# Optimization experiments

Measured on AMD Instinct MI355X. Metric: run time of the kernel, lower is better.

Reference implementation:

```python
import jax, jax.numpy as jnp
import numpy as np

EMB_DIM = 1024
ATT_DIM = 1024
N_HEADS = 16
HEAD_DIM = ATT_DIM // N_HEADS
ROPE_THETA = 10000.0


def setup_inputs() -> dict:
    key = jax.random.key(0)
    k1, k2, k3 = jax.random.split(key, 3)
    B, S = 2, 2048
    x = jax.random.normal(k1, (B, S, EMB_DIM), dtype=jnp.float32)
    # nn.Linear weights stored as [in, out] for x @ W
    W_qkv = jax.random.normal(k2, (EMB_DIM, 3 * ATT_DIM), dtype=jnp.float32) / np.sqrt(EMB_DIM)
    W_out = jax.random.normal(k3, (ATT_DIM, EMB_DIM), dtype=jnp.float32) / np.sqrt(ATT_DIM)
    return {"x": x, "W_qkv": W_qkv, "W_out": W_out}


def _rope_cos_sin(seq_len, dim, dtype):
    # rotary-embedding-torch: freqs over even indices, repeated interleaved
    inv_freq = 1.0 / (ROPE_THETA ** (jnp.arange(0, dim, 2, dtype=jnp.float32) / dim))
    t = jnp.arange(seq_len, dtype=jnp.float32)
    freqs = t[:, None] * inv_freq[None, :]            # [S, dim/2]
    freqs = jnp.repeat(freqs, 2, axis=-1)             # [S, dim] interleaved
    return jnp.cos(freqs).astype(dtype), jnp.sin(freqs).astype(dtype)


def _rotate_half(x):
    # interleaved pairs: (x0, x1) -> (-x1, x0)
    xr = x.reshape(x.shape[:-1] + (x.shape[-1] // 2, 2))
    x1, x2 = xr[..., 0], xr[..., 1]
    return jnp.stack([-x2, x1], axis=-1).reshape(x.shape)


def _apply_rope(x, cos, sin):
    # x: [B, H, S, D]; cos/sin: [S, D]
    return x * cos[None, None] + _rotate_half(x) * sin[None, None]


def reference(x, W_qkv, W_out):
    B, S, _ = x.shape
    qkv = x @ W_qkv                                   # [B, S, 3*ATT]
    qkv = qkv.reshape(B, S, 3, N_HEADS, HEAD_DIM)
    qkv = jnp.moveaxis(qkv, 3, 1)                     # [B, H, S, 3, D]
    q, k, v = qkv[..., 0, :], qkv[..., 1, :], qkv[..., 2, :]

    cos, sin = _rope_cos_sin(S, HEAD_DIM, x.dtype)
    q = _apply_rope(q, cos, sin)
    k = _apply_rope(k, cos, sin)

    scale = 1.0 / np.sqrt(HEAD_DIM)
    scores = jnp.einsum("bhqd,bhkd->bhqk", q, k) * scale
    attn = jax.nn.softmax(scores, axis=-1)
    out = jnp.einsum("bhqk,bhkd->bhqd", attn, v)      # [B, H, S, D]
    out = jnp.moveaxis(out, 1, 2).reshape(B, S, ATT_DIM)
    return out @ W_out                                # [B, S, EMB_DIM]
```

## Files before the change

### kernel.cpp

```cpp
#include <hip/hip_runtime.h>
#include <cstdint>
#include <cstddef>

typedef unsigned short u16;
typedef __bf16 bf16x8 __attribute__((ext_vector_type(8)));
typedef float f32x4 __attribute__((ext_vector_type(4)));
typedef unsigned int u32x4 __attribute__((ext_vector_type(4)));

#define DEVI __device__ __forceinline__

constexpr int SEQ = 2048, NH = 16, HD = 64, EMB = 1024, N3 = 3072, MROWS = 4096;

DEVI u16 f2bf(float f) {
    union { float f; unsigned u; } x; x.f = f;
    unsigned r = (x.u + 0x7fffu + ((x.u >> 16) & 1u)) >> 16;
    return (u16)r;
}

DEVI f32x4 mfma16(bf16x8 a, bf16x8 b, f32x4 c) {
    return __builtin_amdgcn_mfma_f32_16x16x32_bf16(a, b, c, 0, 0, 0);
}

DEVI float exp2_raw(float x) {
    float r;
    asm("v_exp_f32 %0, %1" : "=v"(r) : "v"(x));
    return r;
}

#define GLDS16(g, l)                                                          \
    __builtin_amdgcn_global_load_lds(                                         \
        (__attribute__((address_space(1))) void*)(g),                         \
        (__attribute__((address_space(3))) void*)(l), 16, 0, 0)

#define GWAIT4 asm volatile("s_waitcnt vmcnt(4)" ::: "memory")
#define GWAIT0 asm volatile("s_waitcnt vmcnt(0)" ::: "memory")
#define RBAR                                                                  \
    do {                                                                      \
        __builtin_amdgcn_sched_barrier(0);                                    \
        __builtin_amdgcn_s_barrier();                                         \
        __builtin_amdgcn_sched_barrier(0);                                    \
    } while (0)

__global__ __launch_bounds__(256) void prep_k(const float* __restrict__ x,
                                              const float* __restrict__ wqk,
                                              const float* __restrict__ wo,
                                              u16* __restrict__ xb, u16* __restrict__ wqkvT,
                                              u16* __restrict__ woutT, float2* __restrict__ tab) {
    __shared__ float tile[64][65];
    int bid = blockIdx.x, tid = threadIdx.x;
    if (bid < 4096) {
        int i = bid * 256 + tid;
        float4 v = ((const float4*)x)[i];
        ushort4 o;
        o.x = f2bf(v.x); o.y = f2bf(v.y); o.z = f2bf(v.z); o.w = f2bf(v.w);
        ((ushort4*)xb)[i] = o;
    } else if (bid < 5120) {
        const float* in; u16* out; int N, bx, by;
        if (bid < 4864) { in = wqk; out = wqkvT; N = 3072; int bb = bid - 4096; bx = bb % 48; by = bb / 48; }
        else            { in = wo;  out = woutT; N = 1024; int bb = bid - 4864; bx = bb % 16; by = bb / 16; }
        const int K = 1024;
        int k0 = by * 64, n0 = bx * 64;
        for (int i = 0; i < 16; i++) {
            int idx = i * 256 + tid;
            int r = idx >> 6, c = idx & 63;
            tile[r][c] = in[(size_t)(k0 + r) * N + n0 + c];
        }
        __syncthreads();
        for (int i = 0; i < 16; i++) {
            int idx = i * 256 + tid;
            int n = idx >> 6, k = idx & 63;
            out[(size_t)(n0 + n) * K + k0 + k] = f2bf(tile[k][n]);
        }
    } else {
        int idx = (bid - 5120) * 256 + tid;
        int t = idx >> 5, i = idx & 31;
        double ang = (double)t * pow(10000.0, -(double)i / 32.0);
        tab[idx] = make_float2((float)cos(ang), (float)sin(ang));
    }
}

template <int EPI>
__global__ __launch_bounds__(256, 3) void gemm128_k(const u16* __restrict__ A, const u16* __restrict__ Bt,
                                                    int Kd, int Ncols,
                                                    u16* __restrict__ q_out, u16* __restrict__ k_out,
                                                    u16* __restrict__ v_out,
                                                    const float2* __restrict__ tab,
                                                    float* __restrict__ Cout) {
    __shared__ __align__(16) u16 smem[24576];
    int tid = threadIdx.x, lane = tid & 63, wv = tid >> 6;
    int wr = wv >> 1, wc = wv & 1;
    int l15 = lane & 15, lg = lane >> 4;
    int fr = (l15 >> 1) & 3;

    int nwg = gridDim.x * gridDim.y;
    int bid = blockIdx.y * gridDim.x + blockIdx.x;
    int swzb = (bid & 7) * (nwg >> 3) + (bid >> 3);
    int bx = swzb % gridDim.x, by = swzb / gridDim.x;
    int brow = by * 128, bcol = bx * 128;

    f32x4 acc[4][4];
    for (int i = 0; i < 4; i++)
        for (int j = 0; j < 4; j++) acc[i][j] = (f32x4){0.f, 0.f, 0.f, 0.f};

    const u16* aptr[2];
    const u16* bptr[2];
#pragma unroll
    for (int i = 0; i < 2; i++) {
        int cidx = i * 256 + tid;
        int rrow = cidx >> 2, cc = cidx & 3;
        int sw = (cc ^ ((rrow >> 1) & 3)) * 8;
        aptr[i] = A + (size_t)(brow + rrow) * Kd + sw;
        bptr[i] = Bt + (size_t)(bcol + rrow) * Kd + sw;
    }

    auto stageG = [&](u16* base) {
#pragma unroll
        for (int i = 0; i < 2; i++) {
            GLDS16(aptr[i], base + (i * 256 + tid) * 8);
            GLDS16(bptr[i], base + 4096 + (i * 256 + tid) * 8);
            aptr[i] += 32;
            bptr[i] += 32;
        }
    };

    auto computeT = [&](const u16* base) {
        const u16* Ar = base;
        const u16* Br = base + 4096;
        bf16x8 af[4], bf[4];
#pragma unroll
        for (int mi = 0; mi < 4; mi++)
            af[mi] = *(const bf16x8*)&Ar[(wr * 64 + mi * 16 + l15) * 32 + (lg ^ fr) * 8];
#pragma unroll
        for (int ni = 0; ni < 4; ni++)
            bf[ni] = *(const bf16x8*)&Br[(wc * 64 + ni * 16 + l15) * 32 + (lg ^ fr) * 8];
#pragma unroll
        for (int mi = 0; mi < 4; mi++)
#pragma unroll
            for (int ni = 0; ni < 4; ni++)
                acc[mi][ni] = mfma16(af[mi], bf[ni], acc[mi][ni]);
    };

    u16* b0 = smem;
    u16* b1 = smem + 8192;
    u16* b2 = smem + 16384;

    stageG(b0);
    stageG(b1);
    for (int r = 0; r < 10; ++r) {
        GWAIT4; RBAR; stageG(b2); computeT(b0);
        GWAIT4; RBAR; stageG(b0); computeT(b1);
        GWAIT4; RBAR; stageG(b1); computeT(b2);
    }
    GWAIT4; RBAR; computeT(b0);
    GWAIT0; RBAR; computeT(b1);

    if constexpr (EPI == 0) {
        int c = bcol >> 10;
        int bb = brow >> 11, sbase = brow & 2047;
        int hbase = (bcol & 1023) >> 6;
        if (c == 2) {
            for (int mi = 0; mi < 4; mi++)
                for (int ni = 0; ni < 4; ni++) {
                    int col = wc * 64 + ni * 16 + l15;
                    int d = col & 63, h2 = col >> 6;
                    int s0 = sbase + wr * 64 + mi * 16 + lg * 4;
                    ushort4 pw;
                    pw.x = f2bf(acc[mi][ni][0]);
                    pw.y = f2bf(acc[mi][ni][1]);
                    pw.z = f2bf(acc[mi][ni][2]);
                    pw.w = f2bf(acc[mi][ni][3]);
                    *(ushort4*)&v_out[((size_t)(bb * NH + hbase + h2) * HD + d) * SEQ + s0] = pw;
                }
        } else {
            u16* dst = (c == 0) ? q_out : k_out;
            float sc = (c == 0) ? 0.125f * 1.4426950408889634f : 1.0f;
            u16* ep = smem;
            __syncthreads();
            for (int mi = 0; mi < 4; mi++)
                for (int ni = 0; ni < 4; ni++) {
                    int col = wc * 64 + ni * 16 + l15;
                    int dg = col & 63;
                    for (int r = 0; r < 4; r++) {
                        int rowl = wr * 64 + mi * 16 + lg * 4 + r;
                        int s = sbase + rowl;
                        float val = acc[mi][ni][r];
                        float part = __shfl_xor(val, 1);
                        float2 cs = tab[(s << 5) | (dg >> 1)];
                        float o = (dg & 1) ? (val * cs.x + part * cs.y)
                                           : (val * cs.x - part * cs.y);
                        ep[rowl * 136 + (col ^ ((rowl & 7) << 3))] = f2bf(o * sc);
                    }
                }
            __syncthreads();
#pragma unroll
            for (int p = 0; p < 8; p++) {
                int unit = p * 32 + (tid >> 3);
                int h2 = unit >> 7, s_r = unit & 127, j = tid & 7;
                int cj = (h2 * 8 + j) ^ (s_r & 7);
                uint4 w = *(const uint4*)&ep[s_r * 136 + cj * 8];
                *(uint4*)&dst[(((size_t)(bb * NH + hbase + h2) * SEQ + sbase + s_r) << 6) +
                              j * 8] = w;
            }
        }
    } else {
        for (int mi = 0; mi < 4; mi++)
            for (int ni = 0; ni < 4; ni++) {
                int col = bcol + wc * 64 + ni * 16 + l15;
                for (int r = 0; r < 4; r++) {
                    int row = brow + wr * 64 + mi * 16 + lg * 4 + r;
                    Cout[(size_t)row * Ncols + col] = acc[mi][ni][r];
                }
            }
    }
}

__global__ __launch_bounds__(256, 2) void attn11_k(const u16* __restrict__ Qb,
                                                   const u16* __restrict__ Kb,
                                                   const u16* __restrict__ Vtg,
                                                   u16* __restrict__ Ob) {
    __shared__ __align__(16) u16 Ks[3][64 * 64];
    __shared__ __align__(16) u16 Vs[3][64 * 64];
    int tid = threadIdx.x, lane = tid & 63, wv = tid >> 6;
    int l15 = lane & 15, lg = lane >> 4;
    int fk = (l15 & 3) | (((l15 >> 2) & 1) << 2);
    int fv = (l15 & 3) | (((l15 >> 3) & 1) << 2);
    int bh = blockIdx.y, b = bh >> 4, h = bh & 15;
    int qbase = blockIdx.x * 128;
    const size_t base = (size_t)bh * SEQ * HD;

    int c0 = tid, c1 = 256 + tid;
    int r0 = c0 >> 3, s0 = ((c0 & 7) ^ ((r0 & 3) | ((r0 >> 1) & 4))) * 8;
    int r1 = c1 >> 3, s1 = ((c1 & 7) ^ ((r1 & 3) | ((r1 >> 1) & 4))) * 8;
    const u16* kp0 = Kb + base + r0 * HD + s0;
    const u16* kp1 = Kb + base + r1 * HD + s1;
    const u16* vp0 = Vtg + base + (size_t)r0 * SEQ + s0;
    const u16* vp1 = Vtg + base + (size_t)r1 * SEQ + s1;

    bf16x8 qf[2][2];
#pragma unroll
    for (int u = 0; u < 2; u++)
#pragma unroll
        for (int kt = 0; kt < 2; kt++)
            qf[u][kt] = *(const bf16x8*)&Qb[base + (size_t)(qbase + wv * 32 + u * 16 + l15) * HD +
                                            kt * 32 + lg * 8];

    f32x4 oacc[2][4];
    float Lp[2] = {0.f, 0.f};
#pragma unroll
    for (int u = 0; u < 2; u++)
#pragma unroll
        for (int nt = 0; nt < 4; nt++) oacc[u][nt] = (f32x4){0.f, 0.f, 0.f, 0.f};

    auto stage = [&](u16* Kd, u16* Vd) {
        GLDS16(kp0, Kd + c0 * 8);
        GLDS16(kp1, Kd + c1 * 8);
        GLDS16(vp0, Vd + c0 * 8);
        GLDS16(vp1, Vd + c1 * 8);
        kp0 += 64 * HD; kp1 += 64 * HD;
        vp0 += 64; vp1 += 64;
    };

    auto body = [&](const u16* Kl, const u16* Vl) {
        bf16x8 kf[4][2], vf[4][2];
#pragma unroll
        for (int nt = 0; nt < 4; nt++) {
            int rk = ((nt >> 1) << 5) + ((l15 >> 2) << 3) + ((nt & 1) << 2) + (l15 & 3);
#pragma unroll
            for (int kt = 0; kt < 2; kt++) {
                kf[nt][kt] = *(const bf16x8*)&Kl[rk * 64 + (((kt * 4 + lg) ^ fk)) * 8];
                vf[nt][kt] = *(const bf16x8*)&Vl[(nt * 16 + l15) * 64 +
                                                (((kt * 4 + lg) ^ fv)) * 8];
            }
        }

#pragma unroll
        for (int u = 0; u < 2; u++) {
            f32x4 sa[4];
            __builtin_amdgcn_s_setprio(1);
#pragma unroll
            for (int nt = 0; nt < 4; nt++) {
                f32x4 z = (f32x4){0.f, 0.f, 0.f, 0.f};
#pragma unroll
                for (int kt = 0; kt < 2; kt++) z = mfma16(kf[nt][kt], qf[u][kt], z);
                sa[nt] = z;
            }
            __builtin_amdgcn_s_setprio(0);
            unsigned pk[4][2];
            float ls = 0.f;
#pragma unroll
            for (int nt = 0; nt < 4; nt++) {
                float e0 = exp2_raw(sa[nt][0]), e1 = exp2_raw(sa[nt][1]);
                float e2 = exp2_raw(sa[nt][2]), e3 = exp2_raw(sa[nt][3]);
                ls += (e0 + e1) + (e2 + e3);
                asm("v_cvt_pk_bf16_f32 %0, %1, %2" : "=v"(pk[nt][0]) : "v"(e0), "v"(e1));
                asm("v_cvt_pk_bf16_f32 %0, %1, %2" : "=v"(pk[nt][1]) : "v"(e2), "v"(e3));
            }
            Lp[u] += ls;
            bf16x8 pa[2];
#pragma unroll
            for (int kt = 0; kt < 2; kt++) {
                u32x4 t = {pk[2 * kt][0], pk[2 * kt][1], pk[2 * kt + 1][0], pk[2 * kt + 1][1]};
                pa[kt] = __builtin_bit_cast(bf16x8, t);
            }
            __builtin_amdgcn_s_setprio(1);
#pragma unroll
            for (int kt = 0; kt < 2; kt++)
#pragma unroll
                for (int nt = 0; nt < 4; nt++)
                    oacc[u][nt] = mfma16(pa[kt], vf[nt][kt], oacc[u][nt]);
            __builtin_amdgcn_s_setprio(0);
        }
    };

    stage(Ks[0], Vs[0]);
    stage(Ks[1], Vs[1]);
    for (int r = 0; r < 10; ++r) {
        GWAIT4; RBAR; stage(Ks[2], Vs[2]); body(Ks[0], Vs[0]);
        GWAIT4; RBAR; stage(Ks[0], Vs[0]); body(Ks[1], Vs[1]);
        GWAIT4; RBAR; stage(Ks[1], Vs[1]); body(Ks[2], Vs[2]);
    }
    GWAIT4; RBAR; body(Ks[0], Vs[0]);
    GWAIT0; RBAR; body(Ks[1], Vs[1]);

    float linv[2][4];
#pragma unroll
    for (int u = 0; u < 2; u++) {
        float L = Lp[u];
        L += __shfl_xor(L, 16);
        L += __shfl_xor(L, 32);
#pragma unroll
        for (int r = 0; r < 4; r++) linv[u][r] = 1.0f / __shfl(L, lg * 4 + r);
    }
#pragma unroll
    for (int u = 0; u < 2; u++)
#pragma unroll
        for (int nt = 0; nt < 4; nt++)
#pragma unroll
            for (int r = 0; r < 4; r++) {
                int row = qbase + wv * 32 + u * 16 + lg * 4 + r;
                Ob[(size_t)(b * SEQ + row) * EMB + h * HD + nt * 16 + l15] =
                    f2bf(oacc[u][nt][r] * linv[u][r]);
            }
}


extern "C" void kernel_launch(void* const* d_in, const int* in_sizes, int n_in,
                              void* d_out, int out_size, void* d_ws, size_t ws_size,
                              hipStream_t stream) {
    const float* x = (const float*)d_in[0];
    const float* wqk = (const float*)d_in[1];
    const float* wo = (const float*)d_in[2];
    float* out = (float*)d_out;
    char* ws = (char*)d_ws;

    u16* xb = (u16*)(ws + 0);
    u16* wqkvT = (u16*)(ws + 8388608);
    u16* woutT = (u16*)(ws + 14680064);
    u16* qb = (u16*)(ws + 16777216);
    u16* kb = (u16*)(ws + 25165824);
    u16* vb = (u16*)(ws + 33554432);
    u16* ao = (u16*)(ws + 41943040);
    float2* tab = (float2*)(ws + 50331648);

    prep_k<<<5376, 256, 0, stream>>>(x, wqk, wo, xb, wqkvT, woutT, tab);
    gemm128_k<0><<<dim3(N3 / 128, MROWS / 128), 256, 0, stream>>>(xb, wqkvT, EMB, N3, qb, kb, vb,
                                                                  tab, nullptr);
    attn11_k<<<dim3(SEQ / 128, 2 * NH), 256, 0, stream>>>(qb, kb, vb, ao);
    gemm128_k<1><<<dim3(EMB / 128, MROWS / 128), 256, 0, stream>>>(ao, woutT, EMB, EMB, nullptr,
                                                                   nullptr, nullptr, nullptr, out);
}
```

Measured before the change: 104.7 us.

## Split attention block across eight waves with one 16-row query tile each

The attention kernel now runs 512 threads per block instead of 256. Each of the eight waves handles 16 query rows instead of 32, and each thread stages one K and one V chunk per tile instead of two. The wait counts are adjusted to match. This raises wave-level parallelism and latency hiding and lowers per-thread register use. The cost is that each wave loads K/V fragments from LDS for half as much MFMA work, doubling LDS read traffic per unit of compute, and barriers now span more waves.

```diff
diff --git a/kernel.cpp b/kernel.cpp
--- a/kernel.cpp
+++ b/kernel.cpp
@@ -33,6 +33,7 @@
         (__attribute__((address_space(3))) void*)(l), 16, 0, 0)
 
 #define GWAIT4 asm volatile("s_waitcnt vmcnt(4)" ::: "memory")
+#define GWAIT2 asm volatile("s_waitcnt vmcnt(2)" ::: "memory")
 #define GWAIT0 asm volatile("s_waitcnt vmcnt(0)" ::: "memory")
 #define RBAR                                                                  \
     do {                                                                      \
@@ -214,7 +215,7 @@
     }
 }
 
-__global__ __launch_bounds__(256, 2) void attn11_k(const u16* __restrict__ Qb,
+__global__ __launch_bounds__(512, 2) void attn12_k(const u16* __restrict__ Qb,
                                                    const u16* __restrict__ Kb,
                                                    const u16* __restrict__ Vtg,
                                                    u16* __restrict__ Ob) {
@@ -228,36 +229,26 @@
     int qbase = blockIdx.x * 128;
     const size_t base = (size_t)bh * SEQ * HD;
 
-    int c0 = tid, c1 = 256 + tid;
-    int r0 = c0 >> 3, s0 = ((c0 & 7) ^ ((r0 & 3) | ((r0 >> 1) & 4))) * 8;
-    int r1 = c1 >> 3, s1 = ((c1 & 7) ^ ((r1 & 3) | ((r1 >> 1) & 4))) * 8;
+    int r0 = tid >> 3, s0 = ((tid & 7) ^ ((r0 & 3) | ((r0 >> 1) & 4))) * 8;
     const u16* kp0 = Kb + base + r0 * HD + s0;
-    const u16* kp1 = Kb + base + r1 * HD + s1;
     const u16* vp0 = Vtg + base + (size_t)r0 * SEQ + s0;
-    const u16* vp1 = Vtg + base + (size_t)r1 * SEQ + s1;
-
-    bf16x8 qf[2][2];
-#pragma unroll
-    for (int u = 0; u < 2; u++)
-#pragma unroll
-        for (int kt = 0; kt < 2; kt++)
-            qf[u][kt] = *(const bf16x8*)&Qb[base + (size_t)(qbase + wv * 32 + u * 16 + l15) * HD +
-                                            kt * 32 + lg * 8];
-
-    f32x4 oacc[2][4];
-    float Lp[2] = {0.f, 0.f};
-#pragma unroll
-    for (int u = 0; u < 2; u++)
-#pragma unroll
-        for (int nt = 0; nt < 4; nt++) oacc[u][nt] = (f32x4){0.f, 0.f, 0.f, 0.f};
+
+    bf16x8 qf[2];
+#pragma unroll
+    for (int kt = 0; kt < 2; kt++)
+        qf[kt] = *(const bf16x8*)&Qb[base + (size_t)(qbase + wv * 16 + l15) * HD +
+                                     kt * 32 + lg * 8];
+
+    f32x4 oacc[4];
+    float Lp = 0.f;
+#pragma unroll
+    for (int nt = 0; nt < 4; nt++) oacc[nt] = (f32x4){0.f, 0.f, 0.f, 0.f};
 
     auto stage = [&](u16* Kd, u16* Vd) {
-        GLDS16(kp0, Kd + c0 * 8);
-        GLDS16(kp1, Kd + c1 * 8);
-        GLDS16(vp0, Vd + c0 * 8);
-        GLDS16(vp1, Vd + c1 * 8);
-        kp0 += 64 * HD; kp1 += 64 * HD;
-        vp0 += 64; vp1 += 64;
+        GLDS16(kp0, Kd + tid * 8);
+        GLDS16(vp0, Vd + tid * 8);
+        kp0 += 64 * HD;
+        vp0 += 64;
     };
 
     auto body = [&](const u16* Kl, const u16* Vl) {
@@ -273,74 +264,68 @@
             }
         }
 
-#pragma unroll
-        for (int u = 0; u < 2; u++) {
-            f32x4 sa[4];
-            __builtin_amdgcn_s_setprio(1);
-#pragma unroll
-            for (int nt = 0; nt < 4; nt++) {
-                f32x4 z = (f32x4){0.f, 0.f, 0.f, 0.f};
-#pragma unroll
-                for (int kt = 0; kt < 2; kt++) z = mfma16(kf[nt][kt], qf[u][kt], z);
-                sa[nt] = z;
-            }
-            __builtin_amdgcn_s_setprio(0);
-            unsigned pk[4][2];
-            float ls = 0.f;
-#pragma unroll
-            for (int nt = 0; nt < 4; nt++) {
-                float e0 = exp2_raw(sa[nt][0]), e1 = exp2_raw(sa[nt][1]);
-                float e2 = exp2_raw(sa[nt][2]), e3 = exp2_raw(sa[nt][3]);
-                ls += (e0 + e1) + (e2 + e3);
-                asm("v_cvt_pk_bf16_f32 %0, %1, %2" : "=v"(pk[nt][0]) : "v"(e0), "v"(e1));
-                asm("v_cvt_pk_bf16_f32 %0, %1, %2" : "=v"(pk[nt][1]) : "v"(e2), "v"(e3));
-            }
-            Lp[u] += ls;
-            bf16x8 pa[2];
-#pragma unroll
-            for (int kt = 0; kt < 2; kt++) {
-                u32x4 t = {pk[2 * kt][0], pk[2 * kt][1], pk[2 * kt + 1][0], pk[2 * kt + 1][1]};
-                pa[kt] = __builtin_bit_cast(bf16x8, t);
-            }
-            __builtin_amdgcn_s_setprio(1);
-#pragma unroll
-            for (int kt = 0; kt < 2; kt++)
-#pragma unroll
-                for (int nt = 0; nt < 4; nt++)
-                    oacc[u][nt] = mfma16(pa[kt], vf[nt][kt], oacc[u][nt]);
-            __builtin_amdgcn_s_setprio(0);
-        }
+        f32x4 sa[4];
+        __builtin_amdgcn_s_setprio(1);
+#pragma unroll
+        for (int nt = 0; nt < 4; nt++) {
+            f32x4 z = (f32x4){0.f, 0.f, 0.f, 0.f};
+#pragma unroll
+            for (int kt = 0; kt < 2; kt++) z = mfma16(kf[nt][kt], qf[kt], z);
+            sa[nt] = z;
+        }
+        __builtin_amdgcn_s_setprio(0);
+        unsigned pk[4][2];
+        float ls = 0.f;
+#pragma unroll
+        for (int nt = 0; nt < 4; nt++) {
+            float e0 = exp2_raw(sa[nt][0]), e1 = exp2_raw(sa[nt][1]);
+            float e2 = exp2_raw(sa[nt][2]), e3 = exp2_raw(sa[nt][3]);
+            ls += (e0 + e1) + (e2 + e3);
+            asm("v_cvt_pk_bf16_f32 %0, %1, %2" : "=v"(pk[nt][0]) : "v"(e0), "v"(e1));
+            asm("v_cvt_pk_bf16_f32 %0, %1, %2" : "=v"(pk[nt][1]) : "v"(e2), "v"(e3));
+        }
+        Lp += ls;
+        bf16x8 pa[2];
+#pragma unroll
+        for (int kt = 0; kt < 2; kt++) {
+            u32x4 t = {pk[2 * kt][0], pk[2 * kt][1], pk[2 * kt + 1][0], pk[2 * kt + 1][1]};
+            pa[kt] = __builtin_bit_cast(bf16x8, t);
+        }
+        __builtin_amdgcn_s_setprio(1);
+#pragma unroll
+        for (int kt = 0; kt < 2; kt++)
+#pragma unroll
+            for (int nt = 0; nt < 4; nt++)
+                oacc[nt] = mfma16(pa[kt], vf[nt][kt], oacc[nt]);
+        __builtin_amdgcn_s_setprio(0);
     };
 
     stage(Ks[0], Vs[0]);
     stage(Ks[1], Vs[1]);
     for (int r = 0; r < 10; ++r) {
-        GWAIT4; RBAR; stage(Ks[2], Vs[2]); body(Ks[0], Vs[0]);
-        GWAIT4; RBAR; stage(Ks[0], Vs[0]); body(Ks[1], Vs[1]);
-        GWAIT4; RBAR; stage(Ks[1], Vs[1]); body(Ks[2], Vs[2]);
-    }
-    GWAIT4; RBAR; body(Ks[0], Vs[0]);
+        GWAIT2; RBAR; stage(Ks[2], Vs[2]); body(Ks[0], Vs[0]);
+        GWAIT2; RBAR; stage(Ks[0], Vs[0]); body(Ks[1], Vs[1]);
+        GWAIT2; RBAR; stage(Ks[1], Vs[1]); body(Ks[2], Vs[2]);
+    }
+    GWAIT2; RBAR; body(Ks[0], Vs[0]);
     GWAIT0; RBAR; body(Ks[1], Vs[1]);
 
-    float linv[2][4];
-#pragma unroll
-    for (int u = 0; u < 2; u++) {
-        float L = Lp[u];
+    float linv[4];
+    {
+        float L = Lp;
         L += __shfl_xor(L, 16);
         L += __shfl_xor(L, 32);
 #pragma unroll
-        for (int r = 0; r < 4; r++) linv[u][r] = 1.0f / __shfl(L, lg * 4 + r);
-    }
-#pragma unroll
-    for (int u = 0; u < 2; u++)
-#pragma unroll
-        for (int nt = 0; nt < 4; nt++)
-#pragma unroll
-            for (int r = 0; r < 4; r++) {
-                int row = qbase + wv * 32 + u * 16 + lg * 4 + r;
-                Ob[(size_t)(b * SEQ + row) * EMB + h * HD + nt * 16 + l15] =
-                    f2bf(oacc[u][nt][r] * linv[u][r]);
-            }
+        for (int r = 0; r < 4; r++) linv[r] = 1.0f / __shfl(L, lg * 4 + r);
+    }
+#pragma unroll
+    for (int nt = 0; nt < 4; nt++)
+#pragma unroll
+        for (int r = 0; r < 4; r++) {
+            int row = qbase + wv * 16 + lg * 4 + r;
+            Ob[(size_t)(b * SEQ + row) * EMB + h * HD + nt * 16 + l15] =
+                f2bf(oacc[nt][r] * linv[r]);
+        }
 }
 
 
@@ -365,7 +350,7 @@
     prep_k<<<5376, 256, 0, stream>>>(x, wqk, wo, xb, wqkvT, woutT, tab);
     gemm128_k<0><<<dim3(N3 / 128, MROWS / 128), 256, 0, stream>>>(xb, wqkvT, EMB, N3, qb, kb, vb,
                                                                   tab, nullptr);
-    attn11_k<<<dim3(SEQ / 128, 2 * NH), 256, 0, stream>>>(qb, kb, vb, ao);
+    attn12_k<<<dim3(SEQ / 128, 2 * NH), 512, 0, stream>>>(qb, kb, vb, ao);
     gemm128_k<1><<<dim3(EMB / 128, MROWS / 128), 256, 0, stream>>>(ao, woutT, EMB, EMB, nullptr,
                                                                    nullptr, nullptr, nullptr, out);
 }
```

Result: slower. 119.9 us (+14.5%).

## Split attention KV range across two blocks and merge partial outputs

Applied to the files above, without the earlier changes.

The attention kernel gains a third grid dimension that splits the 2048-key range into two halves. Each half writes its own normalized bf16 output plus its per-row softmax sums, reusing existing workspace regions. A new combine kernel then merges the two halves, weighting each by its share of the total sum. The aim is more parallel blocks and shorter per-block loops, at the cost of an extra kernel launch, extra global traffic and an added bf16 rounding step.

```diff
diff --git a/kernel.cpp b/kernel.cpp
--- a/kernel.cpp
+++ b/kernel.cpp
@@ -15,6 +15,11 @@
     union { float f; unsigned u; } x; x.f = f;
     unsigned r = (x.u + 0x7fffu + ((x.u >> 16) & 1u)) >> 16;
     return (u16)r;
+}
+
+DEVI float bf2f(u16 v) {
+    union { unsigned u; float f; } x; x.u = ((unsigned)v) << 16;
+    return x.f;
 }
 
 DEVI f32x4 mfma16(bf16x8 a, bf16x8 b, f32x4 c) {
@@ -214,10 +219,12 @@
     }
 }
 
-__global__ __launch_bounds__(256, 2) void attn11_k(const u16* __restrict__ Qb,
+__global__ __launch_bounds__(256, 2) void attn14_k(const u16* __restrict__ Qb,
                                                    const u16* __restrict__ Kb,
                                                    const u16* __restrict__ Vtg,
-                                                   u16* __restrict__ Ob) {
+                                                   u16* __restrict__ O0,
+                                                   u16* __restrict__ O1,
+                                                   float* __restrict__ Lf) {
     __shared__ __align__(16) u16 Ks[3][64 * 64];
     __shared__ __align__(16) u16 Vs[3][64 * 64];
     int tid = threadIdx.x, lane = tid & 63, wv = tid >> 6;
@@ -225,16 +232,17 @@
     int fk = (l15 & 3) | (((l15 >> 2) & 1) << 2);
     int fv = (l15 & 3) | (((l15 >> 3) & 1) << 2);
     int bh = blockIdx.y, b = bh >> 4, h = bh & 15;
+    int z = blockIdx.z;
     int qbase = blockIdx.x * 128;
     const size_t base = (size_t)bh * SEQ * HD;
 
     int c0 = tid, c1 = 256 + tid;
     int r0 = c0 >> 3, s0 = ((c0 & 7) ^ ((r0 & 3) | ((r0 >> 1) & 4))) * 8;
     int r1 = c1 >> 3, s1 = ((c1 & 7) ^ ((r1 & 3) | ((r1 >> 1) & 4))) * 8;
-    const u16* kp0 = Kb + base + r0 * HD + s0;
-    const u16* kp1 = Kb + base + r1 * HD + s1;
-    const u16* vp0 = Vtg + base + (size_t)r0 * SEQ + s0;
-    const u16* vp1 = Vtg + base + (size_t)r1 * SEQ + s1;
+    const u16* kp0 = Kb + base + (size_t)(z * 1024 + r0) * HD + s0;
+    const u16* kp1 = Kb + base + (size_t)(z * 1024 + r1) * HD + s1;
+    const u16* vp0 = Vtg + base + (size_t)r0 * SEQ + z * 1024 + s0;
+    const u16* vp1 = Vtg + base + (size_t)r1 * SEQ + z * 1024 + s1;
 
     bf16x8 qf[2][2];
 #pragma unroll
@@ -272,17 +280,16 @@
                                                 (((kt * 4 + lg) ^ fv)) * 8];
             }
         }
-
 #pragma unroll
         for (int u = 0; u < 2; u++) {
             f32x4 sa[4];
             __builtin_amdgcn_s_setprio(1);
 #pragma unroll
             for (int nt = 0; nt < 4; nt++) {
-                f32x4 z = (f32x4){0.f, 0.f, 0.f, 0.f};
-#pragma unroll
-                for (int kt = 0; kt < 2; kt++) z = mfma16(kf[nt][kt], qf[u][kt], z);
-                sa[nt] = z;
+                f32x4 acc0 = (f32x4){0.f, 0.f, 0.f, 0.f};
+#pragma unroll
+                for (int kt = 0; kt < 2; kt++) acc0 = mfma16(kf[nt][kt], qf[u][kt], acc0);
+                sa[nt] = acc0;
             }
             __builtin_amdgcn_s_setprio(0);
             unsigned pk[4][2];
@@ -314,20 +321,25 @@
 
     stage(Ks[0], Vs[0]);
     stage(Ks[1], Vs[1]);
-    for (int r = 0; r < 10; ++r) {
+    for (int r = 0; r < 4; ++r) {
         GWAIT4; RBAR; stage(Ks[2], Vs[2]); body(Ks[0], Vs[0]);
         GWAIT4; RBAR; stage(Ks[0], Vs[0]); body(Ks[1], Vs[1]);
         GWAIT4; RBAR; stage(Ks[1], Vs[1]); body(Ks[2], Vs[2]);
     }
-    GWAIT4; RBAR; body(Ks[0], Vs[0]);
-    GWAIT0; RBAR; body(Ks[1], Vs[1]);
-
+    GWAIT4; RBAR; stage(Ks[2], Vs[2]); body(Ks[0], Vs[0]);
+    GWAIT4; RBAR; stage(Ks[0], Vs[0]); body(Ks[1], Vs[1]);
+    GWAIT4; RBAR; body(Ks[2], Vs[2]);
+    GWAIT0; RBAR; body(Ks[0], Vs[0]);
+
+    u16* dst = (z == 0) ? O0 : O1;
     float linv[2][4];
 #pragma unroll
     for (int u = 0; u < 2; u++) {
         float L = Lp[u];
         L += __shfl_xor(L, 16);
         L += __shfl_xor(L, 32);
+        if (lane < 16)
+            Lf[((size_t)(z * 32 + bh)) * SEQ + qbase + wv * 32 + u * 16 + lane] = L;
 #pragma unroll
         for (int r = 0; r < 4; r++) linv[u][r] = 1.0f / __shfl(L, lg * 4 + r);
     }
@@ -338,9 +350,29 @@
 #pragma unroll
             for (int r = 0; r < 4; r++) {
                 int row = qbase + wv * 32 + u * 16 + lg * 4 + r;
-                Ob[(size_t)(b * SEQ + row) * EMB + h * HD + nt * 16 + l15] =
+                dst[(size_t)(b * SEQ + row) * EMB + h * HD + nt * 16 + l15] =
                     f2bf(oacc[u][nt][r] * linv[u][r]);
             }
+}
+
+__global__ __launch_bounds__(256) void combine_k(u16* __restrict__ O0, const u16* __restrict__ O1,
+                                                 const float* __restrict__ Lf) {
+    int gidx = (blockIdx.x * 256 + threadIdx.x) * 8;
+    int bs = gidx >> 10, emb = gidx & 1023;
+    int b = bs >> 11, s = bs & 2047, h = emb >> 6;
+    int bh = b * NH + h;
+    float L0 = Lf[(size_t)bh * SEQ + s];
+    float L1 = Lf[(size_t)(32 + bh) * SEQ + s];
+    float inv = 1.0f / (L0 + L1);
+    float w0 = L0 * inv, w1 = L1 * inv;
+    uint4 a = *(const uint4*)&O0[gidx];
+    uint4 p = *(const uint4*)&O1[gidx];
+    const u16* au = (const u16*)&a;
+    const u16* pu = (const u16*)&p;
+    u16 out[8];
+#pragma unroll
+    for (int i = 0; i < 8; i++) out[i] = f2bf(bf2f(au[i]) * w0 + bf2f(pu[i]) * w1);
+    *(uint4*)&O0[gidx] = *(uint4*)out;
 }
 
 
@@ -361,11 +393,13 @@
     u16* vb = (u16*)(ws + 33554432);
     u16* ao = (u16*)(ws + 41943040);
     float2* tab = (float2*)(ws + 50331648);
+    float* Lf = (float*)(ws + 8388608);
 
     prep_k<<<5376, 256, 0, stream>>>(x, wqk, wo, xb, wqkvT, woutT, tab);
     gemm128_k<0><<<dim3(N3 / 128, MROWS / 128), 256, 0, stream>>>(xb, wqkvT, EMB, N3, qb, kb, vb,
                                                                   tab, nullptr);
-    attn11_k<<<dim3(SEQ / 128, 2 * NH), 256, 0, stream>>>(qb, kb, vb, ao);
+    attn14_k<<<dim3(SEQ / 128, 2 * NH, 2), 256, 0, stream>>>(qb, kb, vb, ao, xb, Lf);
+    combine_k<<<2048, 256, 0, stream>>>(ao, xb, Lf);
     gemm128_k<1><<<dim3(EMB / 128, MROWS / 128), 256, 0, stream>>>(ao, woutT, EMB, EMB, nullptr,
                                                                    nullptr, nullptr, nullptr, out);
 }
```

Measured after the change: 113.1 us. +8.0%, slower.
